# Kernel optimization log

Hardware: AMD Instinct MI355X
Metric: run time of the kernel (lower is better)

Reference implementation:

```python
import jax, jax.numpy as jnp
import numpy as np
from functools import partial

N_NODES = 50000
N_EDGES = 800000
N_ENT = 100000
N_REL = 500
N_POS = 7            # sub_graph_hop_num + 2
DIM = 128            # node_emb_dim == rel_emb_dim == hidden_dim
HEADS = 8
HEAD_DIM = DIM // HEADS
HOPS = 3             # gnn_hop_num
ALPHA = 0.15
FFN_DIM = 4 * DIM
BATCH = 512
SLOPE = 0.2          # leaky relu negative slope


def _ln(x, g, b):
    mu = jnp.mean(x, axis=-1, keepdims=True)
    var = jnp.var(x, axis=-1, keepdims=True)
    return (x - mu) * jax.lax.rsqrt(var + 1e-5) * g + b


def _gdt_layer(h, src, dst, Wh, ah, at, g1, b1, w1, c1, w2, c2, g2, b2,
               rel_score=None):
    """Graph diffusion-transformer layer: edge-softmax attention + PPR hops."""
    N = h.shape[0]
    f = (h @ Wh).reshape(N, HEADS, HEAD_DIM)          # [N,H,Dh]
    s_src = jnp.sum(f * ah, axis=-1)                  # [N,H]
    s_dst = jnp.sum(f * at, axis=-1)                  # [N,H]
    e = s_src[src] + s_dst[dst]                       # [E,H]
    if rel_score is not None:
        e = e + rel_score
    e = jnp.where(e >= 0, e, SLOPE * e)               # leaky relu
    m = jax.ops.segment_max(e, dst, num_segments=N)   # [N,H]
    m = jnp.where(jnp.isfinite(m), m, 0.0)
    ex = jnp.exp(e - m[dst])
    den = jax.ops.segment_sum(ex, dst, num_segments=N)
    att = ex / (den[dst] + 1e-16)                     # [E,H] edge softmax

    feat0 = f
    def hop(feat, _):
        msg = feat[src] * att[:, :, None]             # [E,H,Dh]
        agg = jax.ops.segment_sum(msg, dst, num_segments=N)
        return ALPHA * feat0 + (1.0 - ALPHA) * agg, None
    feat, _ = jax.lax.scan(hop, feat0, None, length=HOPS)

    o = feat.reshape(N, DIM)
    o = _ln(o + h, g1, b1)                            # residual + LN
    ff = jax.nn.relu(o @ w1 + c1) @ w2 + c2           # FFN
    return _ln(o + ff, g2, b2)


def setup_inputs() -> dict:
    key = jax.random.key(0)
    ks = jax.random.split(key, 32)
    s = 0.05
    inp = {
        'ent_ids': jax.random.randint(ks[0], (N_NODES,), 0, N_ENT),
        'rel_ids': jax.random.randint(ks[1], (N_EDGES,), 0, N_REL),
        'arw_pos': jax.random.randint(ks[2], (N_NODES,), 0, N_POS),
        'src': jax.random.randint(ks[3], (N_EDGES,), 0, N_NODES),
        'dst': jax.random.randint(ks[4], (N_EDGES,), 0, N_NODES),
        'batch_node_ids': jax.random.randint(ks[5], (BATCH,), 0, N_NODES),
        'ent_tab': jax.random.normal(ks[6], (N_ENT, DIM)) * s,
        'rel_tab': jax.random.normal(ks[7], (N_REL, DIM)) * s,
        'pos_tab': jax.random.normal(ks[8], (N_POS, DIM)) * s,
        # layer 0 (RGDT: uses relation features)
        'l0_Wh': jax.random.normal(ks[9], (DIM, DIM)) * s,
        'l0_Wr': jax.random.normal(ks[10], (DIM, DIM)) * s,
        'l0_ah': jax.random.normal(ks[11], (HEADS, HEAD_DIM)) * s,
        'l0_at': jax.random.normal(ks[12], (HEADS, HEAD_DIM)) * s,
        'l0_ar': jax.random.normal(ks[13], (HEADS, HEAD_DIM)) * s,
        'l0_g1': jnp.ones((DIM,)), 'l0_b1': jnp.zeros((DIM,)),
        'l0_w1': jax.random.normal(ks[14], (DIM, FFN_DIM)) * s,
        'l0_c1': jnp.zeros((FFN_DIM,)),
        'l0_w2': jax.random.normal(ks[15], (FFN_DIM, DIM)) * s,
        'l0_c2': jnp.zeros((DIM,)),
        'l0_g2': jnp.ones((DIM,)), 'l0_b2': jnp.zeros((DIM,)),
        # layer 1 (GDT: no relation features)
        'l1_Wh': jax.random.normal(ks[16], (DIM, DIM)) * s,
        'l1_ah': jax.random.normal(ks[17], (HEADS, HEAD_DIM)) * s,
        'l1_at': jax.random.normal(ks[18], (HEADS, HEAD_DIM)) * s,
        'l1_g1': jnp.ones((DIM,)), 'l1_b1': jnp.zeros((DIM,)),
        'l1_w1': jax.random.normal(ks[19], (DIM, FFN_DIM)) * s,
        'l1_c1': jnp.zeros((FFN_DIM,)),
        'l1_w2': jax.random.normal(ks[20], (FFN_DIM, DIM)) * s,
        'l1_c2': jnp.zeros((DIM,)),
        'l1_g2': jnp.ones((DIM,)), 'l1_b2': jnp.zeros((DIM,)),
    }
    return inp


def reference(ent_ids, rel_ids, arw_pos, src, dst, batch_node_ids,
              ent_tab, rel_tab, pos_tab,
              l0_Wh, l0_Wr, l0_ah, l0_at, l0_ar, l0_g1, l0_b1,
              l0_w1, l0_c1, l0_w2, l0_c2, l0_g2, l0_b2,
              l1_Wh, l1_ah, l1_at, l1_g1, l1_b1,
              l1_w1, l1_c1, l1_w2, l1_c2, l1_g2, l1_b2):
    # embedding gathers + positional add
    h = ent_tab[ent_ids] + pos_tab[arw_pos]           # [N,D]
    rel = rel_tab[rel_ids]                            # [E,D]
    # relation contribution to layer-0 attention scores
    fr = (rel @ l0_Wr).reshape(-1, HEADS, HEAD_DIM)
    rel_score = jnp.sum(fr * l0_ar, axis=-1)          # [E,H]
    h = _gdt_layer(h, src, dst, l0_Wh, l0_ah, l0_at, l0_g1, l0_b1,
                   l0_w1, l0_c1, l0_w2, l0_c2, l0_g2, l0_b2,
                   rel_score=rel_score)
    h = _gdt_layer(h, src, dst, l1_Wh, l1_ah, l1_at, l1_g1, l1_b1,
                   l1_w1, l1_c1, l1_w2, l1_c2, l1_g2, l1_b2)
    return h[batch_node_ids]                          # [B,D] cls gather
```

## Files before the change

kernel.cpp:

```cpp
#include <hip/hip_runtime.h>
#include <hip/hip_bf16.h>

#define NNODES 50000
#define NEDGES 800000
#define NP 50048
#define DIM 128
#define HEADS 8
#define FFNDIM 512

typedef __bf16 bf16x8 __attribute__((ext_vector_type(8)));
typedef float f32x4 __attribute__((ext_vector_type(4)));
typedef unsigned int uint32;
typedef unsigned short ushort16;

__device__ __forceinline__ float b2f(uint32 u) {
  union { uint32 i; float f; } x; x.i = u << 16; return x.f;
}
__device__ __forceinline__ ushort16 f2b(float f) {
  __bf16 h = (__bf16)f; return __builtin_bit_cast(ushort16, h);
}

__global__ void k_embed(const int* __restrict__ ent_ids, const int* __restrict__ arw_pos,
                        const float* __restrict__ ent_tab, const float* __restrict__ pos_tab,
                        __bf16* __restrict__ hb) {
  int t = blockIdx.x * 256 + threadIdx.x;
  if (t >= NNODES * 32) return;
  int n = t >> 5, c = t & 31;
  float4 a = ((const float4*)ent_tab)[ent_ids[n] * 32 + c];
  float4 b = ((const float4*)pos_tab)[arw_pos[n] * 32 + c];
  ushort4 o;
  o.x = f2b(a.x + b.x); o.y = f2b(a.y + b.y);
  o.z = f2b(a.z + b.z); o.w = f2b(a.w + b.w);
  ((ushort4*)hb)[t] = o;
}

__global__ void k_wt_all(const float* __restrict__ Wh0, const float* __restrict__ Wh1,
                         const float* __restrict__ w10, const float* __restrict__ w11,
                         const float* __restrict__ w20, const float* __restrict__ w21,
                         __bf16* __restrict__ T0, __bf16* __restrict__ T1,
                         __bf16* __restrict__ T2, __bf16* __restrict__ T3,
                         __bf16* __restrict__ T4, __bf16* __restrict__ T5) {
  int m = blockIdx.y;
  const float* W; __bf16* T; int R, lc;
  switch (m) {
    case 0: W = Wh0; T = T0; R = 128; lc = 7; break;
    case 1: W = Wh1; T = T1; R = 128; lc = 7; break;
    case 2: W = w10; T = T2; R = 128; lc = 9; break;
    case 3: W = w11; T = T3; R = 128; lc = 9; break;
    case 4: W = w20; T = T4; R = 512; lc = 7; break;
    default: W = w21; T = T5; R = 512; lc = 7; break;
  }
  int idx = blockIdx.x * 256 + threadIdx.x;
  if (idx >= (R << lc)) return;
  int r = idx >> lc, c = idx & ((1 << lc) - 1);
  T[(long)c * R + r] = (__bf16)W[idx];
}

__global__ void k_relsc(const float* __restrict__ Wr, const float* __restrict__ ar,
                        const float* __restrict__ rel_tab, float* __restrict__ relsc) {
  __shared__ float vr[1024];
  int tid = threadIdx.x;
  for (int i = tid; i < 1024; i += 256) {
    int d = i >> 3, hh = i & 7;
    float s = 0.f;
    #pragma unroll
    for (int k = 0; k < 16; ++k) s += Wr[d * 128 + hh * 16 + k] * ar[hh * 16 + k];
    vr[i] = s;
  }
  __syncthreads();
  int t = blockIdx.x * 256 + tid;
  if (t >= 500 * 8) return;
  int r = t >> 3, hh = t & 7;
  float s = 0.f;
  for (int d = 0; d < 128; ++d) s += rel_tab[r * 128 + d] * vr[d * 8 + hh];
  relsc[t] = s;
}

__global__ void k_hist(const int* __restrict__ dst, int* __restrict__ deg) {
  int e = blockIdx.x * 256 + threadIdx.x;
  if (e < NEDGES) atomicAdd(&deg[dst[e]], 1);
}

__global__ void k_scan(const int* __restrict__ deg, int* __restrict__ rowptr,
                       int* __restrict__ cursor) {
  __shared__ int wsum[16];
  __shared__ int s_run;
  int tid = threadIdx.x, lane = tid & 63, w = tid >> 6;
  if (tid == 0) s_run = 0;
  __syncthreads();
  for (int base = 0; base < NNODES; base += 1024) {
    int i = base + tid;
    int v = (i < NNODES) ? deg[i] : 0;
    int x = v;
    #pragma unroll
    for (int o = 1; o < 64; o <<= 1) {
      int t = __shfl_up(x, o);
      if (lane >= o) x += t;
    }
    if (lane == 63) wsum[w] = x;
    __syncthreads();
    if (w == 0 && lane < 16) {
      int t = wsum[lane];
      #pragma unroll
      for (int o = 1; o < 16; o <<= 1) {
        int u = __shfl_up(t, o);
        if (lane >= o) t += u;
      }
      wsum[lane] = t;
    }
    __syncthreads();
    int run = s_run;
    int add = run + (w > 0 ? wsum[w - 1] : 0);
    if (i < NNODES) { rowptr[i] = add + x - v; cursor[i] = add + x - v; }
    __syncthreads();
    if (tid == 0) s_run = run + wsum[15];
    __syncthreads();
  }
  if (tid == 0) rowptr[NNODES] = s_run;
}

__global__ void k_scatter(const int* __restrict__ dst, const int* __restrict__ src,
                          const int* __restrict__ rel_ids, int* __restrict__ cursor,
                          uint32* __restrict__ packed) {
  int e = blockIdx.x * 256 + threadIdx.x;
  if (e >= NEDGES) return;
  int p = atomicAdd(&cursor[dst[e]], 1);
  packed[p] = (uint32)src[e] | ((uint32)rel_ids[e] << 16);
}

template<int KDIM, int NB, int EPI>
__global__ __launch_bounds__(256) void k_gemm(
    const __bf16* __restrict__ A, const __bf16* __restrict__ Bt,
    const float* __restrict__ bias, const __bf16* __restrict__ resid,
    __bf16* __restrict__ outb, float* __restrict__ outf) {
  __shared__ char sA[16384];
  __shared__ char sB[16384];
  const int tid = threadIdx.x;
  const int lane = tid & 63, wid = tid >> 6;
  const int wr = wid >> 1, wc = wid & 1;
  const int lr = lane & 15, hi = lane >> 4;
  const long row0 = (long)blockIdx.x * 128;
  const long col0 = (long)blockIdx.y * 128;
  f32x4 acc[4][4] = {};

  for (int kc = 0; kc < KDIM / 64; ++kc) {
    __syncthreads();
    #pragma unroll
    for (int i = 0; i < 4; ++i) {
      int q = i * 256 + tid;
      int r = q >> 3, slot = q & 7;
      int sw = ((slot ^ (r & 7)) << 4);
      int4 av = *(const int4*)(A + (row0 + r) * KDIM + kc * 64 + slot * 8);
      *(int4*)(sA + r * 128 + sw) = av;
      int4 bv = *(const int4*)(Bt + (col0 + r) * KDIM + kc * 64 + slot * 8);
      *(int4*)(sB + r * 128 + sw) = bv;
    }
    __syncthreads();
    #pragma unroll
    for (int ks = 0; ks < 2; ++ks) {
      bf16x8 af[4], bfr[4];
      #pragma unroll
      for (int m = 0; m < 4; ++m) {
        int r = wr * 64 + m * 16 + lr;
        int cb = ((ks * 4 + hi) ^ (r & 7)) << 4;
        af[m] = *(const bf16x8*)(sA + r * 128 + cb);
      }
      #pragma unroll
      for (int n = 0; n < 4; ++n) {
        int r = wc * 64 + n * 16 + lr;
        int cb = ((ks * 4 + hi) ^ (r & 7)) << 4;
        bfr[n] = *(const bf16x8*)(sB + r * 128 + cb);
      }
      #pragma unroll
      for (int m = 0; m < 4; ++m)
        #pragma unroll
        for (int n = 0; n < 4; ++n)
          acc[m][n] = __builtin_amdgcn_mfma_f32_16x16x32_bf16(af[m], bfr[n], acc[m][n], 0, 0, 0);
    }
  }

  #pragma unroll
  for (int m = 0; m < 4; ++m) {
    #pragma unroll
    for (int j = 0; j < 4; ++j) {
      long r = row0 + wr * 64 + m * 16 + hi * 4 + j;
      #pragma unroll
      for (int n = 0; n < 4; ++n) {
        long c = col0 + wc * 64 + n * 16 + lr;
        float v = acc[m][n][j];
        if (EPI == 0) {
          outb[r * NB + c] = (__bf16)v;
        } else if (EPI == 1) {
          outb[r * NB + c] = (__bf16)fmaxf(v + bias[c], 0.f);
        } else {
          outf[r * NB + c] = v + bias[c] + (float)resid[r * NB + c];
        }
      }
    }
  }
}

__global__ void k_scores(const __bf16* __restrict__ f, const float* __restrict__ ah,
                         const float* __restrict__ at, float* __restrict__ ssrc,
                         float* __restrict__ sdst) {
  int lane = threadIdx.x & 63, wid = threadIdx.x >> 6;
  int n = blockIdx.x * 4 + wid;
  if (n >= NNODES) return;
  uint32 v = ((const uint32*)f)[n * 64 + lane];
  float x = b2f(v & 0xffffu), y = b2f(v >> 16);
  float2 a = ((const float2*)ah)[lane];
  float2 t = ((const float2*)at)[lane];
  float ps = x * a.x + y * a.y;
  float pt = x * t.x + y * t.y;
  #pragma unroll
  for (int o = 1; o < 8; o <<= 1) { ps += __shfl_xor(ps, o); pt += __shfl_xor(pt, o); }
  if ((lane & 7) == 0) {
    ssrc[n * 8 + (lane >> 3)] = ps;
    sdst[n * 8 + (lane >> 3)] = pt;
  }
}

__global__ void k_softmax(const int* __restrict__ rowptr, const uint32* __restrict__ packed,
                          const float* __restrict__ ssrc, const float* __restrict__ sdst,
                          const float* __restrict__ relsc, float* __restrict__ att) {
  int lane = threadIdx.x & 63, wid = threadIdx.x >> 6;
  int n = blockIdx.x * 4 + wid;
  if (n >= NNODES) return;
  int start = rowptr[n], end = rowptr[n + 1];
  if (start == end) return;
  int hh = lane & 7, jj = lane >> 3;
  float sd = sdst[n * 8 + hh];
  float m = -1e30f, den = 0.f;
  int deg = end - start;

  if (deg <= 64) {
    uint32 pk[8];
    float ev[8];
    int end1 = end - 1;
    #pragma unroll
    for (int t = 0; t < 8; ++t)
      pk[t] = packed[min(start + t * 8 + jj, end1)];
    #pragma unroll
    for (int t = 0; t < 8; ++t)
      ev[t] = ssrc[(pk[t] & 0xffffu) * 8 + hh];
    #pragma unroll
    for (int t = 0; t < 8; ++t) {
      int j = start + t * 8 + jj;
      float e = ev[t] + sd;
      if (relsc) e += relsc[(pk[t] >> 16) * 8 + hh];
      e = (e >= 0.f) ? e : 0.2f * e;
      ev[t] = e;
      if (j < end) {
        float M = fmaxf(m, e);
        den = den * __expf(m - M) + __expf(e - M);
        m = M;
      }
    }
    #pragma unroll
    for (int o = 8; o < 64; o <<= 1) {
      float m2 = __shfl_xor(m, o), d2 = __shfl_xor(den, o);
      float M = fmaxf(m, m2);
      den = den * __expf(m - M) + d2 * __expf(m2 - M);
      m = M;
    }
    float inv = 1.f / (den + 1e-16f);
    #pragma unroll
    for (int t = 0; t < 8; ++t) {
      int j = start + t * 8 + jj;
      if (j < end) att[j * 8 + hh] = __expf(ev[t] - m) * inv;
    }
  } else {
    for (int j0 = start; j0 < end; j0 += 8) {
      int j = j0 + jj;
      if (j < end) {
        uint32 p2 = packed[j];
        float e = ssrc[(p2 & 0xffffu) * 8 + hh] + sd;
        if (relsc) e += relsc[(p2 >> 16) * 8 + hh];
        e = (e >= 0.f) ? e : 0.2f * e;
        att[j * 8 + hh] = e;
        float M = fmaxf(m, e);
        den = den * __expf(m - M) + __expf(e - M);
        m = M;
      }
    }
    #pragma unroll
    for (int o = 8; o < 64; o <<= 1) {
      float m2 = __shfl_xor(m, o), d2 = __shfl_xor(den, o);
      float M = fmaxf(m, m2);
      den = den * __expf(m - M) + d2 * __expf(m2 - M);
      m = M;
    }
    float inv = 1.f / (den + 1e-16f);
    for (int j0 = start; j0 < end; j0 += 8) {
      int j = j0 + jj;
      if (j < end) {
        float e = att[j * 8 + hh];
        att[j * 8 + hh] = __expf(e - m) * inv;
      }
    }
  }
}

template<int FINAL>
__global__ __launch_bounds__(256) void k_hop(
    const int* __restrict__ rowptr, const uint32* __restrict__ packed,
    const float* __restrict__ att, const __bf16* __restrict__ fin,
    const __bf16* __restrict__ f0, __bf16* __restrict__ fout,
    const __bf16* __restrict__ resid, const float* __restrict__ g,
    const float* __restrict__ b) {
  int lane = threadIdx.x & 63, wid = threadIdx.x >> 6;
  int n = blockIdx.x * 4 + wid;
  if (n >= NNODES) return;
  int start = rowptr[n], end = rowptr[n + 1];
  int hsel = lane >> 3;
  float ax = 0.f, ay = 0.f;
  const uint32* fin2 = (const uint32*)fin;
  if (start < end) {
    int end1 = end - 1;
    int e8 = end * 8 - 1;
    uint32 sv = packed[min(start + (lane & 15), end1)];
    float av0 = att[min(start * 8 + lane, e8)];
    float av1 = att[min(start * 8 + 64 + lane, e8)];
    for (int j0 = start; j0 < end; j0 += 16) {
      uint32 svc = sv; float a0 = av0, a1 = av1;
      int jn = j0 + 16;
      if (jn < end) {
        sv = packed[min(jn + (lane & 15), end1)];
        av0 = att[min(jn * 8 + lane, e8)];
        av1 = att[min(jn * 8 + 64 + lane, e8)];
      }
      #pragma unroll
      for (int k = 0; k < 16; ++k) {
        float a = (k < 8) ? __shfl(a0, k * 8 + hsel) : __shfl(a1, (k - 8) * 8 + hsel);
        a = (j0 + k < end) ? a : 0.f;
        int s = (int)(__shfl(svc, k) & 0xffffu);
        uint32 v = fin2[(long)s * 64 + lane];
        ax += a * b2f(v & 0xffffu);
        ay += a * b2f(v >> 16);
      }
    }
  }
  uint32 z = ((const uint32*)f0)[n * 64 + lane];
  float ox = 0.15f * b2f(z & 0xffffu) + 0.85f * ax;
  float oy = 0.15f * b2f(z >> 16) + 0.85f * ay;
  if (!FINAL) {
    ((uint32*)fout)[n * 64 + lane] = ((uint32)f2b(oy) << 16) | (uint32)f2b(ox);
  } else {
    uint32 rz = ((const uint32*)resid)[n * 64 + lane];
    float x = ox + b2f(rz & 0xffffu);
    float y = oy + b2f(rz >> 16);
    float s = x + y;
    #pragma unroll
    for (int o = 1; o < 64; o <<= 1) s += __shfl_xor(s, o);
    float mean = s * (1.f / 128.f);
    float dx = x - mean, dy = y - mean;
    float q = dx * dx + dy * dy;
    #pragma unroll
    for (int o = 1; o < 64; o <<= 1) q += __shfl_xor(q, o);
    float rs2 = rsqrtf(q * (1.f / 128.f) + 1e-5f);
    float2 gg = ((const float2*)g)[lane];
    float2 bb = ((const float2*)b)[lane];
    float o1 = dx * rs2 * gg.x + bb.x;
    float o2 = dy * rs2 * gg.y + bb.y;
    ((uint32*)fout)[n * 64 + lane] = ((uint32)f2b(o2) << 16) | (uint32)f2b(o1);
  }
}

__global__ void k_ln0(const float* __restrict__ xin, const float* __restrict__ g,
                      const float* __restrict__ b, float* __restrict__ outf,
                      __bf16* __restrict__ outb) {
  int lane = threadIdx.x & 63, wid = threadIdx.x >> 6;
  int n = blockIdx.x * 4 + wid;
  if (n >= NNODES) return;
  float2 v = ((const float2*)xin)[n * 64 + lane];
  float x = v.x, y = v.y;
  float s = x + y;
  #pragma unroll
  for (int o = 1; o < 64; o <<= 1) s += __shfl_xor(s, o);
  float mean = s * (1.f / 128.f);
  float dx = x - mean, dy = y - mean;
  float q = dx * dx + dy * dy;
  #pragma unroll
  for (int o = 1; o < 64; o <<= 1) q += __shfl_xor(q, o);
  float rs = rsqrtf(q * (1.f / 128.f) + 1e-5f);
  float2 gg = ((const float2*)g)[lane];
  float2 bb = ((const float2*)b)[lane];
  float ox = dx * rs * gg.x + bb.x;
  float oy = dy * rs * gg.y + bb.y;
  ((float2*)outf)[n * 64 + lane] = make_float2(ox, oy);
  ((uint32*)outb)[n * 64 + lane] = ((uint32)f2b(oy) << 16) | (uint32)f2b(ox);
}

__global__ void k_gather(const int* __restrict__ ids, const float* __restrict__ h,
                         float* __restrict__ out) {
  int t = blockIdx.x * 256 + threadIdx.x;
  if (t >= 512 * 32) return;
  int b = t >> 5, c = t & 31;
  ((float4*)out)[t] = ((const float4*)h)[(long)ids[b] * 32 + c];
}

struct LayerW {
  const float *Wh, *ah, *at, *g1, *b1, *w1, *c1, *w2, *c2, *g2, *b2;
};

extern "C" void kernel_launch(void* const* d_in, const int* in_sizes, int n_in,
                              void* d_out, int out_size, void* d_ws, size_t ws_size,
                              hipStream_t stream) {
  const int* ent_ids   = (const int*)d_in[0];
  const int* rel_ids   = (const int*)d_in[1];
  const int* arw_pos   = (const int*)d_in[2];
  const int* src       = (const int*)d_in[3];
  const int* dst       = (const int*)d_in[4];
  const int* batch_ids = (const int*)d_in[5];
  const float* ent_tab = (const float*)d_in[6];
  const float* rel_tab = (const float*)d_in[7];
  const float* pos_tab = (const float*)d_in[8];

  LayerW L0 = {(const float*)d_in[9],  (const float*)d_in[11], (const float*)d_in[12],
               (const float*)d_in[14], (const float*)d_in[15], (const float*)d_in[16],
               (const float*)d_in[17], (const float*)d_in[18], (const float*)d_in[19],
               (const float*)d_in[20], (const float*)d_in[21]};
  const float* l0_Wr = (const float*)d_in[10];
  const float* l0_ar = (const float*)d_in[13];
  LayerW L1 = {(const float*)d_in[22], (const float*)d_in[23], (const float*)d_in[24],
               (const float*)d_in[25], (const float*)d_in[26], (const float*)d_in[27],
               (const float*)d_in[28], (const float*)d_in[29], (const float*)d_in[30],
               (const float*)d_in[31], (const float*)d_in[32]};

  char* p = (char*)d_ws;
  auto alloc = [&](size_t bytes) { char* q = p; p += (bytes + 255) & ~(size_t)255; return q; };
  __bf16* hb = (__bf16*)alloc((size_t)NP * 128 * 2);
  __bf16* f  = (__bf16*)alloc((size_t)NP * 128 * 2);
  __bf16* fb = (__bf16*)alloc((size_t)NP * 128 * 2);
  __bf16* fa = (__bf16*)alloc((size_t)NP * 128 * 2);
  __bf16* ob = (__bf16*)alloc((size_t)NP * 128 * 2);
  char*   U  = alloc((size_t)NP * 512 * 2);
  float*  att = (float*)U;
  __bf16* T   = (__bf16*)U;
  float*  y   = (float*)f;
  float* ssrc  = (float*)alloc((size_t)NP * 8 * 4);
  float* sdst  = (float*)alloc((size_t)NP * 8 * 4);
  float* relsc = (float*)alloc(500 * 8 * 4);
  __bf16* Wht0 = (__bf16*)alloc(128 * 128 * 2);
  __bf16* Wht1 = (__bf16*)alloc(128 * 128 * 2);
  __bf16* w1t0 = (__bf16*)alloc(512 * 128 * 2);
  __bf16* w1t1 = (__bf16*)alloc(512 * 128 * 2);
  __bf16* w2t0 = (__bf16*)alloc(128 * 512 * 2);
  __bf16* w2t1 = (__bf16*)alloc(128 * 512 * 2);
  int* deg    = (int*)alloc(NNODES * 4);
  int* rowptr = (int*)alloc((NNODES + 1) * 4);
  int* cursor = (int*)alloc(NNODES * 4);
  uint32* packed = (uint32*)alloc((size_t)NEDGES * 4);

  hipMemsetAsync(hb + (size_t)NNODES * 128, 0, (size_t)(NP - NNODES) * 128 * 2, stream);
  hipMemsetAsync(ob + (size_t)NNODES * 128, 0, (size_t)(NP - NNODES) * 128 * 2, stream);

  k_embed<<<(NNODES * 32 + 255) / 256, 256, 0, stream>>>(ent_ids, arw_pos, ent_tab, pos_tab, hb);
  k_wt_all<<<dim3(256, 6), 256, 0, stream>>>(L0.Wh, L1.Wh, L0.w1, L1.w1, L0.w2, L1.w2,
                                             Wht0, Wht1, w1t0, w1t1, w2t0, w2t1);
  k_relsc<<<16, 256, 0, stream>>>(l0_Wr, l0_ar, rel_tab, relsc);

  hipMemsetAsync(deg, 0, NNODES * sizeof(int), stream);
  k_hist<<<NEDGES / 256, 256, 0, stream>>>(dst, deg);
  k_scan<<<1, 1024, 0, stream>>>(deg, rowptr, cursor);
  k_scatter<<<NEDGES / 256, 256, 0, stream>>>(dst, src, rel_ids, cursor, packed);

  const int NB4 = (NNODES + 3) / 4;
  for (int L = 0; L < 2; ++L) {
    const LayerW& W = L ? L1 : L0;
    const __bf16* Wht = L ? Wht1 : Wht0;
    const __bf16* w1t = L ? w1t1 : w1t0;
    const __bf16* w2t = L ? w2t1 : w2t0;
    const float* rsc  = L ? nullptr : relsc;

    k_gemm<128, 128, 0><<<dim3(391, 1), 256, 0, stream>>>(hb, Wht, nullptr, nullptr, f, nullptr);
    k_scores<<<NB4, 256, 0, stream>>>(f, W.ah, W.at, ssrc, sdst);
    k_softmax<<<NB4, 256, 0, stream>>>(rowptr, packed, ssrc, sdst, rsc, att);
    k_hop<0><<<NB4, 256, 0, stream>>>(rowptr, packed, att, f, f, fa, nullptr, nullptr, nullptr);
    k_hop<0><<<NB4, 256, 0, stream>>>(rowptr, packed, att, fa, f, fb, nullptr, nullptr, nullptr);
    k_hop<1><<<NB4, 256, 0, stream>>>(rowptr, packed, att, fb, f, ob, hb, W.g1, W.b1);
    k_gemm<128, 512, 1><<<dim3(391, 4), 256, 0, stream>>>(ob, w1t, W.c1, nullptr, T, nullptr);
    k_gemm<512, 128, 2><<<dim3(391, 1), 256, 0, stream>>>(T, w2t, W.c2, ob, nullptr, y);
    k_ln0<<<NB4, 256, 0, stream>>>(y, W.g2, W.b2, y, hb);
  }

  k_gather<<<64, 256, 0, stream>>>(batch_ids, y, (float*)d_out);
}
```

Measured before the change: 575.3 us.

## Fuse preprocessing kernels, attention scores into GEMM, LN into FFN GEMM, fp16 attention

```diff
diff --git a/kernel.cpp b/kernel.cpp
--- a/kernel.cpp
+++ b/kernel.cpp
@@ -19,120 +19,202 @@
 __device__ __forceinline__ ushort16 f2b(float f) {
   __bf16 h = (__bf16)f; return __builtin_bit_cast(ushort16, h);
 }
-
-__global__ void k_embed(const int* __restrict__ ent_ids, const int* __restrict__ arw_pos,
-                        const float* __restrict__ ent_tab, const float* __restrict__ pos_tab,
-                        __bf16* __restrict__ hb) {
-  int t = blockIdx.x * 256 + threadIdx.x;
-  if (t >= NNODES * 32) return;
-  int n = t >> 5, c = t & 31;
-  float4 a = ((const float4*)ent_tab)[ent_ids[n] * 32 + c];
-  float4 b = ((const float4*)pos_tab)[arw_pos[n] * 32 + c];
-  ushort4 o;
-  o.x = f2b(a.x + b.x); o.y = f2b(a.y + b.y);
-  o.z = f2b(a.z + b.z); o.w = f2b(a.w + b.w);
-  ((ushort4*)hb)[t] = o;
-}
-
-__global__ void k_wt_all(const float* __restrict__ Wh0, const float* __restrict__ Wh1,
-                         const float* __restrict__ w10, const float* __restrict__ w11,
-                         const float* __restrict__ w20, const float* __restrict__ w21,
-                         __bf16* __restrict__ T0, __bf16* __restrict__ T1,
-                         __bf16* __restrict__ T2, __bf16* __restrict__ T3,
-                         __bf16* __restrict__ T4, __bf16* __restrict__ T5) {
-  int m = blockIdx.y;
-  const float* W; __bf16* T; int R, lc;
-  switch (m) {
-    case 0: W = Wh0; T = T0; R = 128; lc = 7; break;
-    case 1: W = Wh1; T = T1; R = 128; lc = 7; break;
-    case 2: W = w10; T = T2; R = 128; lc = 9; break;
-    case 3: W = w11; T = T3; R = 128; lc = 9; break;
-    case 4: W = w20; T = T4; R = 512; lc = 7; break;
-    default: W = w21; T = T5; R = 512; lc = 7; break;
-  }
-  int idx = blockIdx.x * 256 + threadIdx.x;
-  if (idx >= (R << lc)) return;
-  int r = idx >> lc, c = idx & ((1 << lc) - 1);
-  T[(long)c * R + r] = (__bf16)W[idx];
-}
-
-__global__ void k_relsc(const float* __restrict__ Wr, const float* __restrict__ ar,
-                        const float* __restrict__ rel_tab, float* __restrict__ relsc) {
-  __shared__ float vr[1024];
-  int tid = threadIdx.x;
-  for (int i = tid; i < 1024; i += 256) {
-    int d = i >> 3, hh = i & 7;
+__device__ __forceinline__ float h2f(unsigned short u) {
+  return (float)__builtin_bit_cast(_Float16, u);
+}
+__device__ __forceinline__ unsigned short f2h(float f) {
+  return __builtin_bit_cast(unsigned short, (_Float16)f);
+}
+
+__global__ void k_embed_hist(const int* __restrict__ ent_ids, const int* __restrict__ arw_pos,
+                             const float* __restrict__ ent_tab, const float* __restrict__ pos_tab,
+                             __bf16* __restrict__ hb, const int* __restrict__ dst,
+                             int* __restrict__ deg) {
+  int bid = blockIdx.x, tid = threadIdx.x;
+  if (bid < 6250) {
+    int t = bid * 256 + tid;
+    int n = t >> 5, c = t & 31;
+    float4 a = ((const float4*)ent_tab)[ent_ids[n] * 32 + c];
+    float4 b = ((const float4*)pos_tab)[arw_pos[n] * 32 + c];
+    ushort4 o;
+    o.x = f2b(a.x + b.x); o.y = f2b(a.y + b.y);
+    o.z = f2b(a.z + b.z); o.w = f2b(a.w + b.w);
+    ((ushort4*)hb)[t] = o;
+  } else {
+    int e = (bid - 6250) * 256 + tid;
+    if (e < NEDGES) atomicAdd(&deg[dst[e]], 1);
+  }
+}
+
+__global__ void k_prep(const int* __restrict__ deg, int* __restrict__ rowptr,
+                       int* __restrict__ cursor,
+                       const float* __restrict__ Wr, const float* __restrict__ ar,
+                       const float* __restrict__ rel_tab, float* __restrict__ relsc,
+                       const float* __restrict__ Wh0, const float* __restrict__ Wh1,
+                       const float* __restrict__ w10, const float* __restrict__ w11,
+                       const float* __restrict__ w20, const float* __restrict__ w21,
+                       __bf16* __restrict__ T0, __bf16* __restrict__ T1,
+                       __bf16* __restrict__ T2, __bf16* __restrict__ T3,
+                       __bf16* __restrict__ T4, __bf16* __restrict__ T5) {
+  int bid = blockIdx.x, tid = threadIdx.x;
+  if (bid == 0) {
+    __shared__ int wsum[16];
+    __shared__ int s_run;
+    int lane = tid & 63, w = tid >> 6;
+    if (tid == 0) s_run = 0;
+    __syncthreads();
+    for (int base = 0; base < NNODES; base += 1024) {
+      int i = base + tid;
+      int v = (i < NNODES) ? deg[i] : 0;
+      int x = v;
+      #pragma unroll
+      for (int o = 1; o < 64; o <<= 1) {
+        int t = __shfl_up(x, o);
+        if (lane >= o) x += t;
+      }
+      if (lane == 63) wsum[w] = x;
+      __syncthreads();
+      if (w == 0 && lane < 16) {
+        int t = wsum[lane];
+        #pragma unroll
+        for (int o = 1; o < 16; o <<= 1) {
+          int u = __shfl_up(t, o);
+          if (lane >= o) t += u;
+        }
+        wsum[lane] = t;
+      }
+      __syncthreads();
+      int run = s_run;
+      int add = run + (w > 0 ? wsum[w - 1] : 0);
+      if (i < NNODES) { rowptr[i] = add + x - v; cursor[i] = add + x - v; }
+      __syncthreads();
+      if (tid == 0) s_run = run + wsum[15];
+      __syncthreads();
+    }
+    if (tid == 0) rowptr[NNODES] = s_run;
+  } else if (bid <= 4) {
+    __shared__ float vr[1024];
+    int d = tid >> 3, hh = tid & 7;
     float s = 0.f;
     #pragma unroll
     for (int k = 0; k < 16; ++k) s += Wr[d * 128 + hh * 16 + k] * ar[hh * 16 + k];
-    vr[i] = s;
-  }
-  __syncthreads();
-  int t = blockIdx.x * 256 + tid;
-  if (t >= 500 * 8) return;
-  int r = t >> 3, hh = t & 7;
-  float s = 0.f;
-  for (int d = 0; d < 128; ++d) s += rel_tab[r * 128 + d] * vr[d * 8 + hh];
-  relsc[t] = s;
-}
-
-__global__ void k_hist(const int* __restrict__ dst, int* __restrict__ deg) {
-  int e = blockIdx.x * 256 + threadIdx.x;
-  if (e < NEDGES) atomicAdd(&deg[dst[e]], 1);
-}
-
-__global__ void k_scan(const int* __restrict__ deg, int* __restrict__ rowptr,
-                       int* __restrict__ cursor) {
-  __shared__ int wsum[16];
-  __shared__ int s_run;
-  int tid = threadIdx.x, lane = tid & 63, w = tid >> 6;
-  if (tid == 0) s_run = 0;
-  __syncthreads();
-  for (int base = 0; base < NNODES; base += 1024) {
-    int i = base + tid;
-    int v = (i < NNODES) ? deg[i] : 0;
-    int x = v;
-    #pragma unroll
-    for (int o = 1; o < 64; o <<= 1) {
-      int t = __shfl_up(x, o);
-      if (lane >= o) x += t;
-    }
-    if (lane == 63) wsum[w] = x;
-    __syncthreads();
-    if (w == 0 && lane < 16) {
-      int t = wsum[lane];
-      #pragma unroll
-      for (int o = 1; o < 16; o <<= 1) {
-        int u = __shfl_up(t, o);
-        if (lane >= o) t += u;
-      }
-      wsum[lane] = t;
-    }
-    __syncthreads();
-    int run = s_run;
-    int add = run + (w > 0 ? wsum[w - 1] : 0);
-    if (i < NNODES) { rowptr[i] = add + x - v; cursor[i] = add + x - v; }
-    __syncthreads();
-    if (tid == 0) s_run = run + wsum[15];
-    __syncthreads();
-  }
-  if (tid == 0) rowptr[NNODES] = s_run;
-}
-
-__global__ void k_scatter(const int* __restrict__ dst, const int* __restrict__ src,
-                          const int* __restrict__ rel_ids, int* __restrict__ cursor,
-                          uint32* __restrict__ packed) {
-  int e = blockIdx.x * 256 + threadIdx.x;
-  if (e >= NEDGES) return;
-  int p = atomicAdd(&cursor[dst[e]], 1);
-  packed[p] = (uint32)src[e] | ((uint32)rel_ids[e] << 16);
-}
-
-template<int KDIM, int NB, int EPI>
+    vr[tid] = s;
+    __syncthreads();
+    int t = (bid - 1) * 1024 + tid;
+    if (t < 500 * 8) {
+      int r = t >> 3, h2 = t & 7;
+      float acc = 0.f;
+      for (int dd = 0; dd < 128; ++dd) acc += rel_tab[r * 128 + dd] * vr[dd * 8 + h2];
+      relsc[t] = acc;
+    }
+  } else {
+    int wb = bid - 5;
+    const float* W; __bf16* T; int lc, R;
+    int sub;
+    if (wb < 16)        { W = Wh0; T = T0; lc = 7; R = 128; sub = wb; }
+    else if (wb < 32)   { W = Wh1; T = T1; lc = 7; R = 128; sub = wb - 16; }
+    else if (wb < 96)   { W = w10; T = T2; lc = 9; R = 128; sub = wb - 32; }
+    else if (wb < 160)  { W = w11; T = T3; lc = 9; R = 128; sub = wb - 96; }
+    else if (wb < 224)  { W = w20; T = T4; lc = 7; R = 512; sub = wb - 160; }
+    else                { W = w21; T = T5; lc = 7; R = 512; sub = wb - 224; }
+    int idx = sub * 1024 + tid;
+    int r = idx >> lc, c = idx & ((1 << lc) - 1);
+    T[(long)c * R + r] = (__bf16)W[idx];
+  }
+}
+
+template<int WITH_SCATTER>
+__global__ __launch_bounds__(256) void k_gemm0s(
+    const __bf16* __restrict__ A, const __bf16* __restrict__ Bt,
+    __bf16* __restrict__ fout, const float* __restrict__ ah, const float* __restrict__ at,
+    float* __restrict__ ssrc, float* __restrict__ sdst,
+    const int* __restrict__ dstv, const int* __restrict__ srcv,
+    const int* __restrict__ relv, int* __restrict__ cursor, uint32* __restrict__ packed) {
+  if (WITH_SCATTER && blockIdx.x >= 391) {
+    int e = (blockIdx.x - 391) * 256 + threadIdx.x;
+    if (e < NEDGES) {
+      int p = atomicAdd(&cursor[dstv[e]], 1);
+      packed[p] = (uint32)srcv[e] | ((uint32)relv[e] << 16);
+    }
+    return;
+  }
+  __shared__ char sA[16384];
+  __shared__ char sB[16384];
+  const int tid = threadIdx.x;
+  const int lane = tid & 63, wid = tid >> 6;
+  const int wr = wid >> 1, wc = wid & 1;
+  const int lr = lane & 15, hi = lane >> 4;
+  const long row0 = (long)blockIdx.x * 128;
+  f32x4 acc[4][4] = {};
+
+  for (int kc = 0; kc < 2; ++kc) {
+    __syncthreads();
+    #pragma unroll
+    for (int i = 0; i < 4; ++i) {
+      int q = i * 256 + tid;
+      int r = q >> 3, slot = q & 7;
+      int sw = ((slot ^ (r & 7)) << 4);
+      int4 av = *(const int4*)(A + (row0 + r) * 128 + kc * 64 + slot * 8);
+      *(int4*)(sA + r * 128 + sw) = av;
+      int4 bv = *(const int4*)(Bt + (long)r * 128 + kc * 64 + slot * 8);
+      *(int4*)(sB + r * 128 + sw) = bv;
+    }
+    __syncthreads();
+    #pragma unroll
+    for (int ks = 0; ks < 2; ++ks) {
+      bf16x8 af[4], bfr[4];
+      #pragma unroll
+      for (int m = 0; m < 4; ++m) {
+        int r = wr * 64 + m * 16 + lr;
+        int cb = ((ks * 4 + hi) ^ (r & 7)) << 4;
+        af[m] = *(const bf16x8*)(sA + r * 128 + cb);
+      }
+      #pragma unroll
+      for (int n = 0; n < 4; ++n) {
+        int r = wc * 64 + n * 16 + lr;
+        int cb = ((ks * 4 + hi) ^ (r & 7)) << 4;
+        bfr[n] = *(const bf16x8*)(sB + r * 128 + cb);
+      }
+      #pragma unroll
+      for (int m = 0; m < 4; ++m)
+        #pragma unroll
+        for (int n = 0; n < 4; ++n)
+          acc[m][n] = __builtin_amdgcn_mfma_f32_16x16x32_bf16(af[m], bfr[n], acc[m][n], 0, 0, 0);
+    }
+  }
+
+  float ahr[4], atr[4];
+  #pragma unroll
+  for (int n = 0; n < 4; ++n) {
+    ahr[n] = ah[(wc * 4 + n) * 16 + lr];
+    atr[n] = at[(wc * 4 + n) * 16 + lr];
+  }
+  #pragma unroll
+  for (int m = 0; m < 4; ++m) {
+    #pragma unroll
+    for (int j = 0; j < 4; ++j) {
+      long r = row0 + wr * 64 + m * 16 + hi * 4 + j;
+      #pragma unroll
+      for (int n = 0; n < 4; ++n) {
+        long c = wc * 64 + n * 16 + lr;
+        float v = acc[m][n][j];
+        fout[r * 128 + c] = (__bf16)v;
+        float ps = v * ahr[n], pt = v * atr[n];
+        #pragma unroll
+        for (int o = 1; o < 16; o <<= 1) { ps += __shfl_xor(ps, o); pt += __shfl_xor(pt, o); }
+        if (lr == 0) {
+          ssrc[r * 8 + wc * 4 + n] = ps;
+          sdst[r * 8 + wc * 4 + n] = pt;
+        }
+      }
+    }
+  }
+}
+
+template<int KDIM, int NB>
 __global__ __launch_bounds__(256) void k_gemm(
     const __bf16* __restrict__ A, const __bf16* __restrict__ Bt,
-    const float* __restrict__ bias, const __bf16* __restrict__ resid,
-    __bf16* __restrict__ outb, float* __restrict__ outf) {
+    const float* __restrict__ bias, __bf16* __restrict__ outb) {
   __shared__ char sA[16384];
   __shared__ char sB[16384];
   const int tid = threadIdx.x;
@@ -187,42 +269,109 @@
       #pragma unroll
       for (int n = 0; n < 4; ++n) {
         long c = col0 + wc * 64 + n * 16 + lr;
-        float v = acc[m][n][j];
-        if (EPI == 0) {
-          outb[r * NB + c] = (__bf16)v;
-        } else if (EPI == 1) {
-          outb[r * NB + c] = (__bf16)fmaxf(v + bias[c], 0.f);
-        } else {
-          outf[r * NB + c] = v + bias[c] + (float)resid[r * NB + c];
-        }
-      }
-    }
-  }
-}
-
-__global__ void k_scores(const __bf16* __restrict__ f, const float* __restrict__ ah,
-                         const float* __restrict__ at, float* __restrict__ ssrc,
-                         float* __restrict__ sdst) {
-  int lane = threadIdx.x & 63, wid = threadIdx.x >> 6;
-  int n = blockIdx.x * 4 + wid;
-  if (n >= NNODES) return;
-  uint32 v = ((const uint32*)f)[n * 64 + lane];
-  float x = b2f(v & 0xffffu), y = b2f(v >> 16);
-  float2 a = ((const float2*)ah)[lane];
-  float2 t = ((const float2*)at)[lane];
-  float ps = x * a.x + y * a.y;
-  float pt = x * t.x + y * t.y;
+        outb[r * NB + c] = (__bf16)fmaxf(acc[m][n][j] + bias[c], 0.f);
+      }
+    }
+  }
+}
+
+__global__ __launch_bounds__(256) void k_gemm2ln(
+    const __bf16* __restrict__ A, const __bf16* __restrict__ Bt,
+    const float* __restrict__ bias, const __bf16* __restrict__ resid,
+    const float* __restrict__ g, const float* __restrict__ b,
+    __bf16* __restrict__ outb, float* __restrict__ outf) {
+  __shared__ char smem[65536];
+  char* sA = smem;
+  char* sB = smem + 16384;
+  float* sV = (float*)smem;
+  const int tid = threadIdx.x;
+  const int lane = tid & 63, wid = tid >> 6;
+  const int wr = wid >> 1, wc = wid & 1;
+  const int lr = lane & 15, hi = lane >> 4;
+  const long row0 = (long)blockIdx.x * 128;
+  f32x4 acc[4][4] = {};
+
+  for (int kc = 0; kc < 8; ++kc) {
+    __syncthreads();
+    #pragma unroll
+    for (int i = 0; i < 4; ++i) {
+      int q = i * 256 + tid;
+      int r = q >> 3, slot = q & 7;
+      int sw = ((slot ^ (r & 7)) << 4);
+      int4 av = *(const int4*)(A + (row0 + r) * 512 + kc * 64 + slot * 8);
+      *(int4*)(sA + r * 128 + sw) = av;
+      int4 bv = *(const int4*)(Bt + (long)r * 512 + kc * 64 + slot * 8);
+      *(int4*)(sB + r * 128 + sw) = bv;
+    }
+    __syncthreads();
+    #pragma unroll
+    for (int ks = 0; ks < 2; ++ks) {
+      bf16x8 af[4], bfr[4];
+      #pragma unroll
+      for (int m = 0; m < 4; ++m) {
+        int r = wr * 64 + m * 16 + lr;
+        int cb = ((ks * 4 + hi) ^ (r & 7)) << 4;
+        af[m] = *(const bf16x8*)(sA + r * 128 + cb);
+      }
+      #pragma unroll
+      for (int n = 0; n < 4; ++n) {
+        int r = wc * 64 + n * 16 + lr;
+        int cb = ((ks * 4 + hi) ^ (r & 7)) << 4;
+        bfr[n] = *(const bf16x8*)(sB + r * 128 + cb);
+      }
+      #pragma unroll
+      for (int m = 0; m < 4; ++m)
+        #pragma unroll
+        for (int n = 0; n < 4; ++n)
+          acc[m][n] = __builtin_amdgcn_mfma_f32_16x16x32_bf16(af[m], bfr[n], acc[m][n], 0, 0, 0);
+    }
+  }
+  __syncthreads();
+
+  float biasr[4];
   #pragma unroll
-  for (int o = 1; o < 8; o <<= 1) { ps += __shfl_xor(ps, o); pt += __shfl_xor(pt, o); }
-  if ((lane & 7) == 0) {
-    ssrc[n * 8 + (lane >> 3)] = ps;
-    sdst[n * 8 + (lane >> 3)] = pt;
+  for (int n = 0; n < 4; ++n) biasr[n] = bias[wc * 64 + n * 16 + lr];
+  #pragma unroll
+  for (int m = 0; m < 4; ++m) {
+    #pragma unroll
+    for (int j = 0; j < 4; ++j) {
+      int rloc = wr * 64 + m * 16 + hi * 4 + j;
+      long r = row0 + rloc;
+      #pragma unroll
+      for (int n = 0; n < 4; ++n) {
+        int c = wc * 64 + n * 16 + lr;
+        sV[rloc * 128 + c] = acc[m][n][j] + biasr[n] + (float)resid[r * 128 + c];
+      }
+    }
+  }
+  __syncthreads();
+
+  float2 gg = ((const float2*)g)[lane];
+  float2 bb = ((const float2*)b)[lane];
+  for (int rr = 0; rr < 32; ++rr) {
+    int rloc = wid * 32 + rr;
+    long r = row0 + rloc;
+    float2 v = ((float2*)sV)[rloc * 64 + lane];
+    float x = v.x, y = v.y;
+    float s = x + y;
+    #pragma unroll
+    for (int o = 1; o < 64; o <<= 1) s += __shfl_xor(s, o);
+    float mean = s * (1.f / 128.f);
+    float dx = x - mean, dy = y - mean;
+    float q = dx * dx + dy * dy;
+    #pragma unroll
+    for (int o = 1; o < 64; o <<= 1) q += __shfl_xor(q, o);
+    float rs = rsqrtf(q * (1.f / 128.f) + 1e-5f);
+    float ox = dx * rs * gg.x + bb.x;
+    float oy = dy * rs * gg.y + bb.y;
+    if (outf) ((float2*)outf)[r * 64 + lane] = make_float2(ox, oy);
+    ((uint32*)outb)[r * 64 + lane] = ((uint32)f2b(oy) << 16) | (uint32)f2b(ox);
   }
 }
 
 __global__ void k_softmax(const int* __restrict__ rowptr, const uint32* __restrict__ packed,
                           const float* __restrict__ ssrc, const float* __restrict__ sdst,
-                          const float* __restrict__ relsc, float* __restrict__ att) {
+                          const float* __restrict__ relsc, unsigned short* __restrict__ att16) {
   int lane = threadIdx.x & 63, wid = threadIdx.x >> 6;
   int n = blockIdx.x * 4 + wid;
   if (n >= NNODES) return;
@@ -267,7 +416,7 @@
     #pragma unroll
     for (int t = 0; t < 8; ++t) {
       int j = start + t * 8 + jj;
-      if (j < end) att[j * 8 + hh] = __expf(ev[t] - m) * inv;
+      if (j < end) att16[j * 8 + hh] = f2h(__expf(ev[t] - m) * inv);
     }
   } else {
     for (int j0 = start; j0 < end; j0 += 8) {
@@ -277,7 +426,7 @@
         float e = ssrc[(p2 & 0xffffu) * 8 + hh] + sd;
         if (relsc) e += relsc[(p2 >> 16) * 8 + hh];
         e = (e >= 0.f) ? e : 0.2f * e;
-        att[j * 8 + hh] = e;
+        att16[j * 8 + hh] = f2h(e);
         float M = fmaxf(m, e);
         den = den * __expf(m - M) + __expf(e - M);
         m = M;
@@ -293,10 +442,7 @@
     float inv = 1.f / (den + 1e-16f);
     for (int j0 = start; j0 < end; j0 += 8) {
       int j = j0 + jj;
-      if (j < end) {
-        float e = att[j * 8 + hh];
-        att[j * 8 + hh] = __expf(e - m) * inv;
-      }
+      if (j < end) att16[j * 8 + hh] = f2h(__expf(h2f(att16[j * 8 + hh]) - m) * inv);
     }
   }
 }
@@ -304,7 +450,7 @@
 template<int FINAL>
 __global__ __launch_bounds__(256) void k_hop(
     const int* __restrict__ rowptr, const uint32* __restrict__ packed,
-    const float* __restrict__ att, const __bf16* __restrict__ fin,
+    const unsigned short* __restrict__ att16, const __bf16* __restrict__ fin,
     const __bf16* __restrict__ f0, __bf16* __restrict__ fout,
     const __bf16* __restrict__ resid, const float* __restrict__ g,
     const float* __restrict__ b) {
@@ -312,26 +458,29 @@
   int n = blockIdx.x * 4 + wid;
   if (n >= NNODES) return;
   int start = rowptr[n], end = rowptr[n + 1];
-  int hsel = lane >> 3;
+  int hsel = lane >> 3, hsel2 = lane >> 4, hlo = hsel & 1;
   float ax = 0.f, ay = 0.f;
   const uint32* fin2 = (const uint32*)fin;
+  const uint32* au = (const uint32*)att16;
   if (start < end) {
-    int end1 = end - 1;
-    int e8 = end * 8 - 1;
-    uint32 sv = packed[min(start + (lane & 15), end1)];
-    float av0 = att[min(start * 8 + lane, e8)];
-    float av1 = att[min(start * 8 + 64 + lane, e8)];
-    for (int j0 = start; j0 < end; j0 += 16) {
-      uint32 svc = sv; float a0 = av0, a1 = av1;
-      int jn = j0 + 16;
+    int end1 = end - 1, limit4 = end * 4 - 1;
+    uint32 sv = packed[min(start + (lane & 31), end1)];
+    uint32 a0 = au[min(start * 4 + lane, limit4)];
+    uint32 a1 = au[min(start * 4 + 64 + lane, limit4)];
+    for (int j0 = start; j0 < end; j0 += 32) {
+      uint32 svc = sv, b0 = a0, b1 = a1;
+      int jn = j0 + 32;
       if (jn < end) {
-        sv = packed[min(jn + (lane & 15), end1)];
-        av0 = att[min(jn * 8 + lane, e8)];
-        av1 = att[min(jn * 8 + 64 + lane, e8)];
-      }
-      #pragma unroll
-      for (int k = 0; k < 16; ++k) {
-        float a = (k < 8) ? __shfl(a0, k * 8 + hsel) : __shfl(a1, (k - 8) * 8 + hsel);
+        sv = packed[min(jn + (lane & 31), end1)];
+        a0 = au[min(jn * 4 + lane, limit4)];
+        a1 = au[min(jn * 4 + 64 + lane, limit4)];
+      }
+      #pragma unroll
+      for (int k = 0; k < 32; ++k) {
+        uint32 araw = __shfl((k < 16) ? b0 : b1, ((k & 15) << 2) + hsel2);
+        unsigned short hu = hlo ? (unsigned short)(araw >> 16)
+                                : (unsigned short)(araw & 0xffffu);
+        float a = h2f(hu);
         a = (j0 + k < end) ? a : 0.f;
         int s = (int)(__shfl(svc, k) & 0xffffu);
         uint32 v = fin2[(long)s * 64 + lane];
@@ -364,31 +513,6 @@
     float o2 = dy * rs2 * gg.y + bb.y;
     ((uint32*)fout)[n * 64 + lane] = ((uint32)f2b(o2) << 16) | (uint32)f2b(o1);
   }
-}
-
-__global__ void k_ln0(const float* __restrict__ xin, const float* __restrict__ g,
-                      const float* __restrict__ b, float* __restrict__ outf,
-                      __bf16* __restrict__ outb) {
-  int lane = threadIdx.x & 63, wid = threadIdx.x >> 6;
-  int n = blockIdx.x * 4 + wid;
-  if (n >= NNODES) return;
-  float2 v = ((const float2*)xin)[n * 64 + lane];
-  float x = v.x, y = v.y;
-  float s = x + y;
-  #pragma unroll
-  for (int o = 1; o < 64; o <<= 1) s += __shfl_xor(s, o);
-  float mean = s * (1.f / 128.f);
-  float dx = x - mean, dy = y - mean;
-  float q = dx * dx + dy * dy;
-  #pragma unroll
-  for (int o = 1; o < 64; o <<= 1) q += __shfl_xor(q, o);
-  float rs = rsqrtf(q * (1.f / 128.f) + 1e-5f);
-  float2 gg = ((const float2*)g)[lane];
-  float2 bb = ((const float2*)b)[lane];
-  float ox = dx * rs * gg.x + bb.x;
-  float oy = dy * rs * gg.y + bb.y;
-  ((float2*)outf)[n * 64 + lane] = make_float2(ox, oy);
-  ((uint32*)outb)[n * 64 + lane] = ((uint32)f2b(oy) << 16) | (uint32)f2b(ox);
 }
 
 __global__ void k_gather(const int* __restrict__ ids, const float* __restrict__ h,
@@ -435,7 +559,7 @@
   __bf16* fa = (__bf16*)alloc((size_t)NP * 128 * 2);
   __bf16* ob = (__bf16*)alloc((size_t)NP * 128 * 2);
   char*   U  = alloc((size_t)NP * 512 * 2);
-  float*  att = (float*)U;
+  unsigned short* att16 = (unsigned short*)U;
   __bf16* T   = (__bf16*)U;
   float*  y   = (float*)f;
   float* ssrc  = (float*)alloc((size_t)NP * 8 * 4);
@@ -454,16 +578,12 @@
 
   hipMemsetAsync(hb + (size_t)NNODES * 128, 0, (size_t)(NP - NNODES) * 128 * 2, stream);
   hipMemsetAsync(ob + (size_t)NNODES * 128, 0, (size_t)(NP - NNODES) * 128 * 2, stream);
-
-  k_embed<<<(NNODES * 32 + 255) / 256, 256, 0, stream>>>(ent_ids, arw_pos, ent_tab, pos_tab, hb);
-  k_wt_all<<<dim3(256, 6), 256, 0, stream>>>(L0.Wh, L1.Wh, L0.w1, L1.w1, L0.w2, L1.w2,
-                                             Wht0, Wht1, w1t0, w1t1, w2t0, w2t1);
-  k_relsc<<<16, 256, 0, stream>>>(l0_Wr, l0_ar, rel_tab, relsc);
-
   hipMemsetAsync(deg, 0, NNODES * sizeof(int), stream);
-  k_hist<<<NEDGES / 256, 256, 0, stream>>>(dst, deg);
-  k_scan<<<1, 1024, 0, stream>>>(deg, rowptr, cursor);
-  k_scatter<<<NEDGES / 256, 256, 0, stream>>>(dst, src, rel_ids, cursor, packed);
+
+  k_embed_hist<<<9375, 256, 0, stream>>>(ent_ids, arw_pos, ent_tab, pos_tab, hb, dst, deg);
+  k_prep<<<293, 1024, 0, stream>>>(deg, rowptr, cursor, l0_Wr, l0_ar, rel_tab, relsc,
+                                   L0.Wh, L1.Wh, L0.w1, L1.w1, L0.w2, L1.w2,
+                                   Wht0, Wht1, w1t0, w1t1, w2t0, w2t1);
 
   const int NB4 = (NNODES + 3) / 4;
   for (int L = 0; L < 2; ++L) {
@@ -473,15 +593,20 @@
     const __bf16* w2t = L ? w2t1 : w2t0;
     const float* rsc  = L ? nullptr : relsc;
 
-    k_gemm<128, 128, 0><<<dim3(391, 1), 256, 0, stream>>>(hb, Wht, nullptr, nullptr, f, nullptr);
-    k_scores<<<NB4, 256, 0, stream>>>(f, W.ah, W.at, ssrc, sdst);
-    k_softmax<<<NB4, 256, 0, stream>>>(rowptr, packed, ssrc, sdst, rsc, att);
-    k_hop<0><<<NB4, 256, 0, stream>>>(rowptr, packed, att, f, f, fa, nullptr, nullptr, nullptr);
-    k_hop<0><<<NB4, 256, 0, stream>>>(rowptr, packed, att, fa, f, fb, nullptr, nullptr, nullptr);
-    k_hop<1><<<NB4, 256, 0, stream>>>(rowptr, packed, att, fb, f, ob, hb, W.g1, W.b1);
-    k_gemm<128, 512, 1><<<dim3(391, 4), 256, 0, stream>>>(ob, w1t, W.c1, nullptr, T, nullptr);
-    k_gemm<512, 128, 2><<<dim3(391, 1), 256, 0, stream>>>(T, w2t, W.c2, ob, nullptr, y);
-    k_ln0<<<NB4, 256, 0, stream>>>(y, W.g2, W.b2, y, hb);
+    if (L == 0) {
+      k_gemm0s<1><<<391 + 3125, 256, 0, stream>>>(hb, Wht, f, W.ah, W.at, ssrc, sdst,
+                                                  dst, src, rel_ids, cursor, packed);
+    } else {
+      k_gemm0s<0><<<391, 256, 0, stream>>>(hb, Wht, f, W.ah, W.at, ssrc, sdst,
+                                           nullptr, nullptr, nullptr, nullptr, nullptr);
+    }
+    k_softmax<<<NB4, 256, 0, stream>>>(rowptr, packed, ssrc, sdst, rsc, att16);
+    k_hop<0><<<NB4, 256, 0, stream>>>(rowptr, packed, att16, f, f, fa, nullptr, nullptr, nullptr);
+    k_hop<0><<<NB4, 256, 0, stream>>>(rowptr, packed, att16, fa, f, fb, nullptr, nullptr, nullptr);
+    k_hop<1><<<NB4, 256, 0, stream>>>(rowptr, packed, att16, fb, f, ob, hb, W.g1, W.b1);
+    k_gemm<128, 512><<<dim3(391, 4), 256, 0, stream>>>(ob, w1t, W.c1, T);
+    k_gemm2ln<<<391, 256, 0, stream>>>(T, w2t, W.c2, ob, W.g2, W.b2, hb,
+                                       (L == 1) ? y : nullptr);
   }
 
   k_gather<<<64, 256, 0, stream>>>(batch_ids, y, (float*)d_out);
```

New measurement: 605.9 us. 5.3% more time.
